# Performance work log

Measured on AMD Instinct MI355X. Metric: run time of the kernel, lower is better.

## Reference

```python
import jax, jax.numpy as jnp
import numpy as np

B, S, DIM, H, D = 2, 2048, 1024, 16, 64
WINDOW = 512
MAX_MEM_SEGMENTS = 1
ROPE_THETA = 10000.0


def _rope(t, pos):
    # lucidrains rotary-embedding-torch default: interleaved pairs
    d = t.shape[-1]
    inv_freq = 1.0 / (ROPE_THETA ** (jnp.arange(0, d, 2, dtype=jnp.float32) / d))
    freqs = pos[:, None].astype(jnp.float32) * inv_freq[None, :]        # [S, d/2]
    freqs = jnp.repeat(freqs, 2, axis=-1)                               # [S, d]
    cos, sin = jnp.cos(freqs), jnp.sin(freqs)
    t1, t2 = t[..., 0::2], t[..., 1::2]
    rot = jnp.stack((-t2, t1), axis=-1).reshape(t.shape)                # rotate_half
    return t * cos + rot * sin


def setup_inputs() -> dict:
    key = jax.random.key(0)
    ks = jax.random.split(key, 8)
    tokens = jax.random.normal(ks[0], (B, S, DIM), dtype=jnp.float32)
    value_residual = jax.random.normal(ks[1], (B, H, S, D), dtype=jnp.float32)
    episode_ids = jnp.sort(jax.random.randint(ks[2], (B, S), 0, 4), axis=-1)
    w = 0.02
    Wq = jax.random.normal(ks[3], (DIM, H * D), dtype=jnp.float32) * w
    Wkv = jax.random.normal(ks[4], (DIM, 2 * H * D), dtype=jnp.float32) * w
    Wo = jax.random.normal(ks[5], (H * D, DIM), dtype=jnp.float32) * w
    Wg = jax.random.normal(ks[6], (DIM, H), dtype=jnp.float32) * w
    Wmix = jax.random.normal(ks[7], (DIM, H), dtype=jnp.float32) * w
    return {"tokens": tokens, "value_residual": value_residual, "episode_ids": episode_ids,
            "Wq": Wq, "Wkv": Wkv, "Wo": Wo, "Wg": Wg, "Wmix": Wmix}


def reference(tokens, value_residual, episode_ids, Wq, Wkv, Wo, Wg, Wmix):
    b, s, _ = tokens.shape
    scale = D ** -0.5

    def split_heads(x):  # [b, n, h*d] -> [b, h, n, d]
        return x.reshape(b, s, H, D).transpose(0, 2, 1, 3)

    q = split_heads(tokens @ Wq)
    kv = tokens @ Wkv
    k, v = split_heads(kv[..., :H * D]), split_heads(kv[..., H * D:])

    q = q * scale

    # value-residual lerp: v.lerp(value_residual, mix)
    mix = jax.nn.sigmoid(jnp.einsum('bnd,dh->bhn', tokens, Wmix))[..., None]  # [b,h,n,1]
    v = v + mix * (value_residual - v)

    pos = jnp.arange(s)
    q = _rope(q, pos)
    k = _rope(k, pos)

    sim = jnp.einsum('bhid,bhjd->bhij', q, k)

    # fixed-window causal mask: masked where dist < 0 or dist > max_mem_segments*window
    dist = pos[:, None] - pos[None, :]
    win_mask = (dist < 0) | (dist > MAX_MEM_SEGMENTS * WINDOW)            # [s, s]
    ep_mask = episode_ids[:, :, None] != episode_ids[:, None, :]          # [b, s, s]
    mask = win_mask[None, None, :, :] | ep_mask[:, None, :, :]

    sim = jnp.where(mask, -jnp.finfo(sim.dtype).max, sim)
    attn = jax.nn.softmax(sim, axis=-1)
    out = jnp.einsum('bhij,bhjd->bhid', attn, v)

    # sigmoid value gating
    gate = jax.nn.sigmoid(jnp.einsum('bnd,dh->bhn', tokens, Wg))[..., None]
    out = out * gate

    out = out.transpose(0, 2, 1, 3).reshape(b, s, H * D)
    return out @ Wo
```

## Files before the change

### kernel.cpp

```cpp
#include <hip/hip_runtime.h>
#include <math.h>

#define BB 2
#define SS 2048
#define DIMM 1024
#define HH 16
#define DD 64
#define WINDOW 512

typedef __bf16 bf16x8 __attribute__((ext_vector_type(8)));
typedef __bf16 bf16x4 __attribute__((ext_vector_type(4)));
typedef float f32x4 __attribute__((ext_vector_type(4)));

__device__ __forceinline__ unsigned short f2bf(float f) {
    unsigned int u = __float_as_uint(f);
    u = (u + 0x7FFFu + ((u >> 16) & 1u)) >> 16;
    return (unsigned short)u;
}
__device__ __forceinline__ float bf2f(unsigned short u) {
    return __uint_as_float((unsigned int)u << 16);
}

__device__ __forceinline__ void async_cp16(unsigned short* lds_dst, const unsigned short* g_src) {
    __builtin_amdgcn_global_load_lds(
        (const __attribute__((address_space(1))) unsigned int*)g_src,
        (__attribute__((address_space(3))) unsigned int*)lds_dst, 16, 0, 0);
}

__global__ __launch_bounds__(256) void prep_kernel(
    const float* __restrict__ tokens, unsigned short* __restrict__ tokA,
    const float* __restrict__ Wg, const float* __restrict__ Wmix,
    unsigned short* __restrict__ wgmt,
    const int* __restrict__ ep, int* __restrict__ epstart)
{
    int bid = blockIdx.x;
    int tid = threadIdx.x;
    if (bid < 2048) {
        const int n4 = (BB * SS * DIMM) / 4;
        for (int i = bid * 256 + tid; i < n4; i += 2048 * 256) {
            float4 v = ((const float4*)tokens)[i];
            ushort4 o;
            o.x = f2bf(v.x); o.y = f2bf(v.y); o.z = f2bf(v.z); o.w = f2bf(v.w);
            ((ushort4*)tokA)[i] = o;
        }
    } else if (bid < 2176) {
        int idx = (bid - 2048) * 256 + tid;
        int n = idx >> 10, k = idx & 1023;
        const float* src = (n < 16) ? Wg : Wmix;
        wgmt[idx] = f2bf(src[k * HH + (n & 15)]);
    } else {
        int idx = (bid - 2176) * 256 + tid;
        int b = idx >> 11, i = idx & 2047;
        const int* e = ep + b * SS;
        int v = e[i];
        int lo = 0, hi = i;
        while (lo < hi) {
            int mid = (lo + hi) >> 1;
            if (e[mid] == v) hi = mid; else lo = mid + 1;
        }
        epstart[idx] = lo;
    }
}

__global__ __launch_bounds__(256) void transpose_cvt3_kernel(
    const float* __restrict__ Wq, const float* __restrict__ Wkv,
    const float* __restrict__ Wo, unsigned short* __restrict__ BtW,
    unsigned short* __restrict__ WotW)
{
    int z = blockIdx.z;
    const float* src = (z == 0) ? Wq : (z == 1) ? Wkv : Wo;
    unsigned short* dst = (z == 0) ? BtW : (z == 1) ? (BtW + 1024 * 1024) : WotW;
    int C = (z == 1) ? 2048 : 1024;
    if (blockIdx.x * 32 >= C) return;
    const int R = 1024;

    __shared__ float t[32][33];
    int c0 = blockIdx.x * 32, r0 = blockIdx.y * 32;
    int tx = threadIdx.x & 31, ty = threadIdx.x >> 5;
    #pragma unroll
    for (int u = 0; u < 4; ++u)
        t[ty + 8 * u][tx] = src[(size_t)(r0 + ty + 8 * u) * C + c0 + tx];
    __syncthreads();
    #pragma unroll
    for (int u = 0; u < 4; ++u)
        dst[(size_t)(c0 + ty + 8 * u) * R + r0 + tx] = f2bf(t[tx][ty + 8 * u]);
}

__global__ __launch_bounds__(256) void mixgate_mfma(
    const unsigned short* __restrict__ A,
    const unsigned short* __restrict__ Bt,
    float* __restrict__ gate, float* __restrict__ mix)
{
    int mbase = blockIdx.x * 16;
    int tid = threadIdx.x;
    int wave = tid >> 6, lane = tid & 63;
    int fr = lane & 15, hi = lane >> 4;
    int kw = wave * 256;

    __shared__ float red[4][16][32];

    f32x4 acc[2];
    acc[0] = (f32x4){0.f, 0.f, 0.f, 0.f};
    acc[1] = (f32x4){0.f, 0.f, 0.f, 0.f};

    const unsigned short* a0 = A + (size_t)(mbase + fr) * 1024 + kw + hi * 8;
    const unsigned short* b0 = Bt + (size_t)fr * 1024 + kw + hi * 8;
    const unsigned short* b1 = Bt + (size_t)(16 + fr) * 1024 + kw + hi * 8;

    #pragma unroll 2
    for (int k = 0; k < 256; k += 32) {
        bf16x8 af0 = *(const bf16x8*)(a0 + k);
        bf16x8 bf0 = *(const bf16x8*)(b0 + k);
        bf16x8 bf1 = *(const bf16x8*)(b1 + k);
        acc[0] = __builtin_amdgcn_mfma_f32_16x16x32_bf16(af0, bf0, acc[0], 0, 0, 0);
        acc[1] = __builtin_amdgcn_mfma_f32_16x16x32_bf16(af0, bf1, acc[1], 0, 0, 0);
    }

    #pragma unroll
    for (int n_ = 0; n_ < 2; ++n_)
        #pragma unroll
        for (int j = 0; j < 4; ++j)
            red[wave][hi * 4 + j][n_ * 16 + fr] = acc[n_][j];
    __syncthreads();

    #pragma unroll
    for (int e = 0; e < 2; ++e) {
        int idx = tid * 2 + e;
        int r = idx >> 5, c = idx & 31;
        float s4 = red[0][r][c] + red[1][r][c] + red[2][r][c] + red[3][r][c];
        float sg = 1.f / (1.f + __expf(-s4));
        int mg = mbase + r;
        int b = mg >> 11, s = mg & 2047;
        int h = c & 15;
        float* dst = (c < 16) ? gate : mix;
        dst[((size_t)b * HH + h) * SS + s] = sg;
    }
}

template<int EPI, int BM, int BN>
__global__ __launch_bounds__(256) void gemm_mfma(
    const unsigned short* __restrict__ A, const unsigned short* __restrict__ Bt,
    void* __restrict__ o0v, void* __restrict__ o1v, void* __restrict__ o2v)
{
    const int K = 1024;
    constexpr int MFR = BM / 32;
    constexpr int NFR = BN / 32;
    int nbase = blockIdx.x * BN;
    int mbase = blockIdx.y * BM;

    int tid = threadIdx.x;
    int lane = tid & 63;
    int wave = tid >> 6;
    int wr = wave >> 1, wc = wave & 1;
    int fr = lane & 15, hi = lane >> 4;

    __shared__ unsigned short As[2][BM * 32];
    __shared__ unsigned short Bs[2][BN * 32];

    int srow = tid >> 2;
    int sp   = tid & 3;
    int scol = (sp ^ ((srow >> 1) & 3)) * 8;
    const unsigned short* agp0 = A  + (size_t)(mbase + srow) * K + scol;
    const unsigned short* agp1 = (BM == 128)
        ? A + (size_t)(mbase + srow + 64) * K + scol : agp0;
    const unsigned short* bgp0 = Bt + (size_t)(nbase + srow) * K + scol;
    const unsigned short* bgp1 = (BN == 128)
        ? Bt + (size_t)(nbase + srow + 64) * K + scol : bgp0;

    f32x4 acc[MFR][NFR];
    #pragma unroll
    for (int m_ = 0; m_ < MFR; ++m_)
        #pragma unroll
        for (int n_ = 0; n_ < NFR; ++n_)
            acc[m_][n_] = (f32x4){0.f, 0.f, 0.f, 0.f};

    int aidx[MFR], bidx[NFR];
    #pragma unroll
    for (int m_ = 0; m_ < MFR; ++m_) {
        int row = wr * (BM / 2) + m_ * 16 + fr;
        aidx[m_] = row * 32 + (hi ^ ((row >> 1) & 3)) * 8;
    }
    #pragma unroll
    for (int n_ = 0; n_ < NFR; ++n_) {
        int row = wc * (BN / 2) + n_ * 16 + fr;
        bidx[n_] = row * 32 + (hi ^ ((row >> 1) & 3)) * 8;
    }

    auto stage = [&](int buf, int k0) {
        async_cp16(&As[buf][tid * 8], agp0 + k0);
        if constexpr (BM == 128)
            async_cp16(&As[buf][2048 + tid * 8], agp1 + k0);
        async_cp16(&Bs[buf][tid * 8], bgp0 + k0);
        if constexpr (BN == 128)
            async_cp16(&Bs[buf][2048 + tid * 8], bgp1 + k0);
    };

    stage(0, 0);
    for (int k0 = 0; k0 < K; k0 += 32) {
        int cur = (k0 >> 5) & 1;
        __syncthreads();
        if (k0 + 32 < K) stage(cur ^ 1, k0 + 32);

        bf16x8 af[MFR], bfr[NFR];
        #pragma unroll
        for (int m_ = 0; m_ < MFR; ++m_) af[m_] = *(const bf16x8*)&As[cur][aidx[m_]];
        #pragma unroll
        for (int n_ = 0; n_ < NFR; ++n_) bfr[n_] = *(const bf16x8*)&Bs[cur][bidx[n_]];
        #pragma unroll
        for (int m_ = 0; m_ < MFR; ++m_)
            #pragma unroll
            for (int n_ = 0; n_ < NFR; ++n_)
                acc[m_][n_] = __builtin_amdgcn_mfma_f32_16x16x32_bf16(
                    af[m_], bfr[n_], acc[m_][n_], 0, 0, 0);
    }

    #pragma unroll
    for (int m_ = 0; m_ < MFR; ++m_) {
        #pragma unroll
        for (int n_ = 0; n_ < NFR; ++n_) {
            int c = nbase + wc * (BN / 2) + n_ * 16 + fr;
            #pragma unroll
            for (int j = 0; j < 4; ++j) {
                int mg = mbase + wr * (BM / 2) + m_ * 16 + hi * 4 + j;
                float v = acc[m_][n_][j];
                if (EPI == 0) {
                    ((float*)o0v)[(size_t)mg * 1024 + c] = v;
                } else {
                    int b = mg >> 11, s = mg & 2047;
                    int cc = c & 1023, h = cc >> 6, d = cc & 63;
                    unsigned short* dst = (c < 1024) ? (unsigned short*)o0v
                                        : (c < 2048) ? (unsigned short*)o1v
                                                     : (unsigned short*)o2v;
                    dst[(((size_t)b * HH + h) * SS + s) * DD + d] = f2bf(v);
                }
            }
        }
    }
}

__global__ __launch_bounds__(256) void rope_lerp_kernel(
    unsigned short* __restrict__ q, unsigned short* __restrict__ k,
    const unsigned short* __restrict__ v0, const float* __restrict__ vres,
    const float* __restrict__ mix, unsigned short* __restrict__ vt)
{
    int st = blockIdx.x;
    int bh = blockIdx.y;
    int tid = threadIdx.x;
    int sl = tid >> 2;
    int dg = (tid & 3) * 16;
    int s = st * 64 + sl;
    size_t rowoff = ((size_t)bh * SS + s) * DD + dg;

    __shared__ unsigned short vtile[64][66];

    union { uint4 v[2]; unsigned short u[16]; } qa, ka, va;
    qa.v[0] = *(const uint4*)(q + rowoff);
    qa.v[1] = *(const uint4*)(q + rowoff + 8);
    ka.v[0] = *(const uint4*)(k + rowoff);
    ka.v[1] = *(const uint4*)(k + rowoff + 8);
    va.v[0] = *(const uint4*)(v0 + rowoff);
    va.v[1] = *(const uint4*)(v0 + rowoff + 8);
    float4 w[4];
    #pragma unroll
    for (int u = 0; u < 4; ++u) w[u] = *(const float4*)(vres + rowoff + 4 * u);
    float mx = mix[(size_t)bh * SS + s];

    #pragma unroll
    for (int u = 0; u < 8; ++u) {
        int d0 = dg + 2 * u;
        float inv_freq = powf(10000.f, -(float)d0 * (1.f / 64.f));
        float fr = (float)s * inv_freq;
        float red = fr - 6.2831853f * floorf(fr * 0.15915494f);
        float cs, sn;
        __sincosf(red, &sn, &cs);
        float x = bf2f(qa.u[2 * u]), y = bf2f(qa.u[2 * u + 1]);
        qa.u[2 * u]     = f2bf((x * cs - y * sn) * 0.125f);
        qa.u[2 * u + 1] = f2bf((y * cs + x * sn) * 0.125f);
        x = bf2f(ka.u[2 * u]); y = bf2f(ka.u[2 * u + 1]);
        ka.u[2 * u]     = f2bf(x * cs - y * sn);
        ka.u[2 * u + 1] = f2bf(y * cs + x * sn);
    }
    *(uint4*)(q + rowoff)     = qa.v[0];
    *(uint4*)(q + rowoff + 8) = qa.v[1];
    *(uint4*)(k + rowoff)     = ka.v[0];
    *(uint4*)(k + rowoff + 8) = ka.v[1];

    #pragma unroll
    for (int e = 0; e < 16; ++e) {
        float vv = bf2f(va.u[e]);
        float wr = ((const float*)w)[e];
        vtile[sl][dg + e] = f2bf(vv + mx * (wr - vv));
    }
    __syncthreads();

    int d = tid >> 2;
    int sseg = (tid & 3) * 16;
    union { uint4 v[2]; unsigned short u[16]; } ot;
    #pragma unroll
    for (int e = 0; e < 16; ++e) ot.u[e] = vtile[sseg + e][d];
    unsigned short* dst = vt + ((size_t)bh * DD + d) * SS + st * 64 + sseg;
    *(uint4*)dst = ot.v[0];
    *(uint4*)(dst + 8) = ot.v[1];
}

__global__ __launch_bounds__(256) void attn_mfma(
    const unsigned short* __restrict__ qbh, const unsigned short* __restrict__ kbh,
    const unsigned short* __restrict__ vt, const int* __restrict__ epstart,
    const float* __restrict__ gate, unsigned short* __restrict__ ao)
{
    int orig = blockIdx.x;
    int swz  = (orig & 7) * 128 + (orig >> 3);
    int bh = swz >> 5, qt = swz & 31;
    int b = bh >> 4, h = bh & 15;
    int q0 = qt * 64;
    int tid = threadIdx.x;
    int wave = tid >> 6, lane = tid & 63;
    int lq = lane & 15, lg = lane >> 4;
    int i = q0 + wave * 16 + lq;

    __shared__ unsigned short Ks[4096];
    __shared__ unsigned short Vs[4096];
    alignas(16) __shared__ unsigned short P_lds[4][16][72];

    int srow0 = tid >> 3, sch = tid & 7;
    int srow1 = srow0 + 32;
    int sc0 = ((sch ^ (srow0 & 7)) << 3);
    int sc1 = ((sch ^ (srow1 & 7)) << 3);
    const unsigned short* kS0 = kbh + ((size_t)bh * SS + srow0) * DD + sc0;
    const unsigned short* kS1 = kbh + ((size_t)bh * SS + srow1) * DD + sc1;
    const unsigned short* vS0 = vt + ((size_t)bh * DD + srow0) * SS + sc0;
    const unsigned short* vS1 = vt + ((size_t)bh * DD + srow1) * SS + sc1;

    int fidx[4];
    #pragma unroll
    for (int n = 0; n < 4; ++n) {
        int r = 16 * n + lq;
        fidx[n] = r * 64 + ((lg ^ (r & 7)) << 3);
    }

    const unsigned short* qrow = qbh + ((size_t)bh * SS + i) * DD + lg * 8;
    bf16x8 bq0 = *(const bf16x8*)qrow;
    bf16x8 bq1 = *(const bf16x8*)(qrow + 32);

    int jmin = i - WINDOW;
    int es = epstart[b * SS + i];
    if (es > jmin) jmin = es;
    float gi = gate[(size_t)bh * SS + i];

    float m = -1e30f, l = 0.f;
    f32x4 o[4];
    #pragma unroll
    for (int n = 0; n < 4; ++n) o[n] = (f32x4){0.f, 0.f, 0.f, 0.f};

    int t0 = (qt < 8) ? (8 - qt) : 0;
    int nt = 9 - t0;
    int jb0 = 64 * (qt - 8 + t0);

    for (int u = 0; u < nt; ++u) {
        int jbase = jb0 + 64 * u;

        __syncthreads();
        async_cp16(&Ks[tid * 8],        kS0 + (size_t)jbase * DD);
        async_cp16(&Ks[2048 + tid * 8], kS1 + (size_t)jbase * DD);
        async_cp16(&Vs[tid * 8],        vS0 + jbase);
        async_cp16(&Vs[2048 + tid * 8], vS1 + jbase);
        __syncthreads();

        f32x4 acc[4];
        #pragma unroll
        for (int n = 0; n < 4; ++n) acc[n] = (f32x4){0.f, 0.f, 0.f, 0.f};
        __builtin_amdgcn_s_setprio(1);
        #pragma unroll
        for (int n = 0; n < 4; ++n) {
            bf16x8 kf0 = *(const bf16x8*)&Ks[fidx[n]];
            bf16x8 kf1 = *(const bf16x8*)&Ks[fidx[n] ^ 32];
            acc[n] = __builtin_amdgcn_mfma_f32_16x16x32_bf16(kf0, bq0, acc[n], 0, 0, 0);
            acc[n] = __builtin_amdgcn_mfma_f32_16x16x32_bf16(kf1, bq1, acc[n], 0, 0, 0);
        }
        __builtin_amdgcn_s_setprio(0);

        int jb = jbase + lg * 4;
        #pragma unroll
        for (int n = 0; n < 4; ++n)
            #pragma unroll
            for (int r = 0; r < 4; ++r) {
                int j = jb + 16 * n + r;
                if (j < jmin || j > i) acc[n][r] = -3e38f;
            }

        float tm = -3e38f;
        #pragma unroll
        for (int n = 0; n < 4; ++n)
            tm = fmaxf(tm, fmaxf(fmaxf(acc[n][0], acc[n][1]), fmaxf(acc[n][2], acc[n][3])));
        tm = fmaxf(tm, __shfl_xor(tm, 16, 64));
        tm = fmaxf(tm, __shfl_xor(tm, 32, 64));
        float mnew = fmaxf(m, tm);
        float scale = __expf(m - mnew);
        float ts = 0.f;
        #pragma unroll
        for (int n = 0; n < 4; ++n)
            #pragma unroll
            for (int r = 0; r < 4; ++r) {
                float p = __expf(acc[n][r] - mnew);
                acc[n][r] = p;
                ts += p;
            }
        ts += __shfl_xor(ts, 16, 64);
        ts += __shfl_xor(ts, 32, 64);
        l = l * scale + ts;
        m = mnew;
        #pragma unroll
        for (int n = 0; n < 4; ++n) o[n] = o[n] * scale;

        #pragma unroll
        for (int n = 0; n < 4; ++n) {
            bf16x4 pv;
            pv[0] = (__bf16)acc[n][0]; pv[1] = (__bf16)acc[n][1];
            pv[2] = (__bf16)acc[n][2]; pv[3] = (__bf16)acc[n][3];
            *(bf16x4*)&P_lds[wave][lq][16 * n + lg * 4] = pv;
        }
        bf16x8 bp0 = *(const bf16x8*)&P_lds[wave][lq][lg * 8];
        bf16x8 bp1 = *(const bf16x8*)&P_lds[wave][lq][32 + lg * 8];

        __builtin_amdgcn_s_setprio(1);
        #pragma unroll
        for (int n = 0; n < 4; ++n) {
            bf16x8 vf0 = *(const bf16x8*)&Vs[fidx[n]];
            bf16x8 vf1 = *(const bf16x8*)&Vs[fidx[n] ^ 32];
            o[n] = __builtin_amdgcn_mfma_f32_16x16x32_bf16(vf0, bp0, o[n], 0, 0, 0);
            o[n] = __builtin_amdgcn_mfma_f32_16x16x32_bf16(vf1, bp1, o[n], 0, 0, 0);
        }
        __builtin_amdgcn_s_setprio(0);
    }

    float g = gi / l;
    #pragma unroll
    for (int n = 0; n < 4; ++n) {
        bf16x4 ov;
        ov[0] = (__bf16)(o[n][0] * g); ov[1] = (__bf16)(o[n][1] * g);
        ov[2] = (__bf16)(o[n][2] * g); ov[3] = (__bf16)(o[n][3] * g);
        *(bf16x4*)(ao + (((size_t)b * SS + i) * HH + h) * DD + 16 * n + lg * 4) = ov;
    }
}

extern "C" void kernel_launch(void* const* d_in, const int* in_sizes, int n_in,
                              void* d_out, int out_size, void* d_ws, size_t ws_size,
                              hipStream_t stream)
{
    const float* tokens = (const float*)d_in[0];
    const float* vres   = (const float*)d_in[1];
    const int*   ep     = (const int*)d_in[2];
    const float* Wq     = (const float*)d_in[3];
    const float* Wkv    = (const float*)d_in[4];
    const float* Wo     = (const float*)d_in[5];
    const float* Wg     = (const float*)d_in[6];
    const float* Wmix   = (const float*)d_in[7];
    float* out = (float*)d_out;

    char* wsb = (char*)d_ws;
    unsigned short* qbh  = (unsigned short*)(wsb + 0);
    unsigned short* kbh  = (unsigned short*)(wsb + 8388608);
    unsigned short* vb0  = (unsigned short*)(wsb + 16777216);
    unsigned short* vtb  = (unsigned short*)(wsb + 25165824);
    unsigned short* aob  = (unsigned short*)(wsb + 33554432);
    unsigned short* tokA = (unsigned short*)(wsb + 41943040);
    unsigned short* BtW  = (unsigned short*)(wsb + 50331648);
    float* gatep = (float*)(wsb + 56623104);
    float* mixp  = (float*)(wsb + 56885248);
    int*   epst  = (int*)(wsb + 57147392);
    unsigned short* wgmt = (unsigned short*)(wsb + 57163776);
    unsigned short* WotW = (unsigned short*)(wsb + 57229312);

    prep_kernel<<<2192, 256, 0, stream>>>(tokens, tokA, Wg, Wmix, wgmt, ep, epst);
    transpose_cvt3_kernel<<<dim3(64, 32, 3), 256, 0, stream>>>(Wq, Wkv, Wo, BtW, WotW);

    mixgate_mfma<<<256, 256, 0, stream>>>(tokA, wgmt, gatep, mixp);
    gemm_mfma<1, 128, 128><<<dim3(24, 32), 256, 0, stream>>>(tokA, BtW, qbh, kbh, vb0);
    rope_lerp_kernel<<<dim3(SS / 64, BB * HH), 256, 0, stream>>>(qbh, kbh, vb0, vres, mixp, vtb);
    attn_mfma<<<1024, 256, 0, stream>>>(qbh, kbh, vtb, epst, gatep, aob);

    gemm_mfma<0, 128, 64><<<dim3(16, 32), 256, 0, stream>>>(aob, WotW, out, nullptr, nullptr);
}
```

Measured before the change: 117.8 us.

## Add dedicated 256x256-tile QKV projection GEMM with swizzled LDS and block remap

Replaces the generic 128x128 GEMM for the QKV projection with a specialized 512-thread kernel that uses 256x256 output tiles, K-steps of 64, and an XOR-swizzled LDS layout to avoid bank conflicts. It also remaps block indices so neighbouring blocks share operand tiles in cache, and double-buffers async global-to-LDS loads with explicit vmcnt waits. The generic GEMM loses its QKV epilogue and is kept only for the output projection. Larger tiles raise data reuse but launch only 192 blocks and use about 128KB of LDS and many accumulator registers, which may cut occupancy and leave some compute units idle on a 256-CU part.

```diff
diff --git a/kernel.cpp b/kernel.cpp
--- a/kernel.cpp
+++ b/kernel.cpp
@@ -137,10 +137,117 @@
     }
 }
 
-template<int EPI, int BM, int BN>
+__global__ __launch_bounds__(512) void gemm_proj256(
+    const unsigned short* __restrict__ A, const unsigned short* __restrict__ Bt,
+    unsigned short* __restrict__ q, unsigned short* __restrict__ kbuf,
+    unsigned short* __restrict__ v)
+{
+    const int K = 1024;
+    const int NT = 16;
+
+    int lin = blockIdx.y * 12 + blockIdx.x;
+    int swz = (lin & 7) * 24 + (lin >> 3);
+    int nbase = (swz % 12) * 256;
+    int mbase = (swz / 12) * 256;
+
+    int tid = threadIdx.x;
+    int lane = tid & 63;
+    int wave = tid >> 6;
+    int wr = wave >> 2, wc = wave & 3;
+    int fr = lane & 15, hi = lane >> 4;
+
+    __shared__ unsigned short As[2][256 * 64];
+    __shared__ unsigned short Bs[2][256 * 64];
+
+    int srow_in = tid >> 3;
+    int g_ch = (lane & 7) ^ (lane >> 3);
+
+    auto stage = [&](int buf, int kt) {
+        int k0 = kt * 64;
+        #pragma unroll
+        for (int s = 0; s < 4; ++s) {
+            int row = s * 64 + srow_in;
+            async_cp16(&As[buf][s * 4096 + tid * 8],
+                       A + (size_t)(mbase + row) * K + k0 + g_ch * 8);
+        }
+        #pragma unroll
+        for (int s = 0; s < 4; ++s) {
+            int row = s * 64 + srow_in;
+            async_cp16(&Bs[buf][s * 4096 + tid * 8],
+                       Bt + (size_t)(nbase + row) * K + k0 + g_ch * 8);
+        }
+    };
+
+    f32x4 acc[8][4];
+    #pragma unroll
+    for (int mf = 0; mf < 8; ++mf)
+        #pragma unroll
+        for (int nf = 0; nf < 4; ++nf)
+            acc[mf][nf] = (f32x4){0.f, 0.f, 0.f, 0.f};
+
+    int sofs0 = ((0 * 4 + hi) ^ (fr & 7)) * 8;
+    int sofs1 = ((1 * 4 + hi) ^ (fr & 7)) * 8;
+    int arow0 = (wr * 128 + fr) * 64;
+    int brow0 = (wc * 64 + fr) * 64;
+
+    auto compute = [&](int buf) {
+        #pragma unroll
+        for (int ks = 0; ks < 2; ++ks) {
+            int so = ks ? sofs1 : sofs0;
+            bf16x8 bfr[4];
+            #pragma unroll
+            for (int nf = 0; nf < 4; ++nf)
+                bfr[nf] = *(const bf16x8*)&Bs[buf][brow0 + nf * 1024 + so];
+            #pragma unroll
+            for (int mf = 0; mf < 8; ++mf) {
+                bf16x8 af = *(const bf16x8*)&As[buf][arow0 + mf * 1024 + so];
+                #pragma unroll
+                for (int nf = 0; nf < 4; ++nf)
+                    acc[mf][nf] = __builtin_amdgcn_mfma_f32_16x16x32_bf16(
+                        af, bfr[nf], acc[mf][nf], 0, 0, 0);
+            }
+        }
+    };
+
+    stage(0, 0);
+    stage(1, 1);
+    for (int kt = 0; kt < NT; kt += 2) {
+        if (kt + 1 < NT) asm volatile("s_waitcnt vmcnt(8)" ::: "memory");
+        else             asm volatile("s_waitcnt vmcnt(0)" ::: "memory");
+        __builtin_amdgcn_s_barrier();
+        compute(0);
+        __builtin_amdgcn_s_barrier();
+        if (kt + 2 < NT) stage(0, kt + 2);
+
+        if (kt + 2 < NT) asm volatile("s_waitcnt vmcnt(8)" ::: "memory");
+        else             asm volatile("s_waitcnt vmcnt(0)" ::: "memory");
+        __builtin_amdgcn_s_barrier();
+        compute(1);
+        __builtin_amdgcn_s_barrier();
+        if (kt + 3 < NT) stage(1, kt + 3);
+    }
+
+    #pragma unroll
+    for (int mf = 0; mf < 8; ++mf) {
+        #pragma unroll
+        for (int nf = 0; nf < 4; ++nf) {
+            int c = nbase + wc * 64 + nf * 16 + fr;
+            int cc = c & 1023, h = cc >> 6, d = cc & 63;
+            unsigned short* dst = (c < 1024) ? q : (c < 2048) ? kbuf : v;
+            #pragma unroll
+            for (int j = 0; j < 4; ++j) {
+                int mg = mbase + wr * 128 + mf * 16 + hi * 4 + j;
+                int b = mg >> 11, s = mg & 2047;
+                dst[(((size_t)b * HH + h) * SS + s) * DD + d] = f2bf(acc[mf][nf][j]);
+            }
+        }
+    }
+}
+
+template<int BM, int BN>
 __global__ __launch_bounds__(256) void gemm_mfma(
     const unsigned short* __restrict__ A, const unsigned short* __restrict__ Bt,
-    void* __restrict__ o0v, void* __restrict__ o1v, void* __restrict__ o2v)
+    float* __restrict__ C)
 {
     const int K = 1024;
     constexpr int MFR = BM / 32;
@@ -222,17 +329,7 @@
             #pragma unroll
             for (int j = 0; j < 4; ++j) {
                 int mg = mbase + wr * (BM / 2) + m_ * 16 + hi * 4 + j;
-                float v = acc[m_][n_][j];
-                if (EPI == 0) {
-                    ((float*)o0v)[(size_t)mg * 1024 + c] = v;
-                } else {
-                    int b = mg >> 11, s = mg & 2047;
-                    int cc = c & 1023, h = cc >> 6, d = cc & 63;
-                    unsigned short* dst = (c < 1024) ? (unsigned short*)o0v
-                                        : (c < 2048) ? (unsigned short*)o1v
-                                                     : (unsigned short*)o2v;
-                    dst[(((size_t)b * HH + h) * SS + s) * DD + d] = f2bf(v);
-                }
+                C[(size_t)mg * 1024 + c] = acc[m_][n_][j];
             }
         }
     }
@@ -475,9 +572,9 @@
     transpose_cvt3_kernel<<<dim3(64, 32, 3), 256, 0, stream>>>(Wq, Wkv, Wo, BtW, WotW);
 
     mixgate_mfma<<<256, 256, 0, stream>>>(tokA, wgmt, gatep, mixp);
-    gemm_mfma<1, 128, 128><<<dim3(24, 32), 256, 0, stream>>>(tokA, BtW, qbh, kbh, vb0);
+    gemm_proj256<<<dim3(12, 16), 512, 0, stream>>>(tokA, BtW, qbh, kbh, vb0);
     rope_lerp_kernel<<<dim3(SS / 64, BB * HH), 256, 0, stream>>>(qbh, kbh, vb0, vres, mixp, vtb);
     attn_mfma<<<1024, 256, 0, stream>>>(qbh, kbh, vtb, epst, gatep, aob);
 
-    gemm_mfma<0, 128, 64><<<dim3(16, 32), 256, 0, stream>>>(aob, WotW, out, nullptr, nullptr);
-}
+    gemm_mfma<128, 64><<<dim3(16, 32), 256, 0, stream>>>(aob, WotW, out);
+}
```

Result: no change. 118.5 us (+0.6%).

## Merge prep kernels, fuse mix/gate into QKV GEMM, widen attention blocks

Applied to the files above, without the earlier changes.

Folds the weight transpose/convert kernel into the token prep kernel, and merges the mix/gate projection into the QKV projection GEMM launch as extra blocks. This cuts two kernel launches and lets the small mixgate work fill idle slots next to the GEMM tiles. Attention blocks grow to 128 query rows with 512 threads, so each K/V tile loaded into LDS is shared by twice as many queries, at the cost of fewer blocks and a wider causal key range per block.

```diff
diff --git a/kernel.cpp b/kernel.cpp
--- a/kernel.cpp
+++ b/kernel.cpp
@@ -27,29 +27,56 @@
         (__attribute__((address_space(3))) unsigned int*)lds_dst, 16, 0, 0);
 }
 
-__global__ __launch_bounds__(256) void prep_kernel(
+__global__ __launch_bounds__(256) void prep_all_kernel(
     const float* __restrict__ tokens, unsigned short* __restrict__ tokA,
+    const float* __restrict__ Wq, const float* __restrict__ Wkv,
+    const float* __restrict__ Wo, unsigned short* __restrict__ BtW,
+    unsigned short* __restrict__ WotW,
     const float* __restrict__ Wg, const float* __restrict__ Wmix,
     unsigned short* __restrict__ wgmt,
     const int* __restrict__ ep, int* __restrict__ epstart)
 {
     int bid = blockIdx.x;
     int tid = threadIdx.x;
-    if (bid < 2048) {
+    if (bid < 4096) {
+        const float* src;
+        unsigned short* dst;
+        int C, bx, by;
+        if (bid < 1024) {
+            src = Wq; dst = BtW; C = 1024; bx = bid & 31; by = bid >> 5;
+        } else if (bid < 3072) {
+            int rel = bid - 1024;
+            src = Wkv; dst = BtW + 1024 * 1024; C = 2048; bx = rel & 63; by = rel >> 6;
+        } else {
+            int rel = bid - 3072;
+            src = Wo; dst = WotW; C = 1024; bx = rel & 31; by = rel >> 5;
+        }
+        const int R = 1024;
+        __shared__ float t[32][33];
+        int c0 = bx * 32, r0 = by * 32;
+        int tx = tid & 31, ty = tid >> 5;
+        #pragma unroll
+        for (int u = 0; u < 4; ++u)
+            t[ty + 8 * u][tx] = src[(size_t)(r0 + ty + 8 * u) * C + c0 + tx];
+        __syncthreads();
+        #pragma unroll
+        for (int u = 0; u < 4; ++u)
+            dst[(size_t)(c0 + ty + 8 * u) * R + r0 + tx] = f2bf(t[tx][ty + 8 * u]);
+    } else if (bid < 6144) {
         const int n4 = (BB * SS * DIMM) / 4;
-        for (int i = bid * 256 + tid; i < n4; i += 2048 * 256) {
+        for (int i = (bid - 4096) * 256 + tid; i < n4; i += 2048 * 256) {
             float4 v = ((const float4*)tokens)[i];
             ushort4 o;
             o.x = f2bf(v.x); o.y = f2bf(v.y); o.z = f2bf(v.z); o.w = f2bf(v.w);
             ((ushort4*)tokA)[i] = o;
         }
-    } else if (bid < 2176) {
-        int idx = (bid - 2048) * 256 + tid;
+    } else if (bid < 6272) {
+        int idx = (bid - 6144) * 256 + tid;
         int n = idx >> 10, k = idx & 1023;
         const float* src = (n < 16) ? Wg : Wmix;
         wgmt[idx] = f2bf(src[k * HH + (n & 15)]);
     } else {
-        int idx = (bid - 2176) * 256 + tid;
+        int idx = (bid - 6272) * 256 + tid;
         int b = idx >> 11, i = idx & 2047;
         const int* e = ep + b * SS;
         int v = e[i];
@@ -62,85 +89,144 @@
     }
 }
 
-__global__ __launch_bounds__(256) void transpose_cvt3_kernel(
-    const float* __restrict__ Wq, const float* __restrict__ Wkv,
-    const float* __restrict__ Wo, unsigned short* __restrict__ BtW,
-    unsigned short* __restrict__ WotW)
-{
-    int z = blockIdx.z;
-    const float* src = (z == 0) ? Wq : (z == 1) ? Wkv : Wo;
-    unsigned short* dst = (z == 0) ? BtW : (z == 1) ? (BtW + 1024 * 1024) : WotW;
-    int C = (z == 1) ? 2048 : 1024;
-    if (blockIdx.x * 32 >= C) return;
-    const int R = 1024;
-
-    __shared__ float t[32][33];
-    int c0 = blockIdx.x * 32, r0 = blockIdx.y * 32;
-    int tx = threadIdx.x & 31, ty = threadIdx.x >> 5;
-    #pragma unroll
-    for (int u = 0; u < 4; ++u)
-        t[ty + 8 * u][tx] = src[(size_t)(r0 + ty + 8 * u) * C + c0 + tx];
-    __syncthreads();
-    #pragma unroll
-    for (int u = 0; u < 4; ++u)
-        dst[(size_t)(c0 + ty + 8 * u) * R + r0 + tx] = f2bf(t[tx][ty + 8 * u]);
-}
-
-__global__ __launch_bounds__(256) void mixgate_mfma(
-    const unsigned short* __restrict__ A,
-    const unsigned short* __restrict__ Bt,
+__global__ __launch_bounds__(256) void projmix_kernel(
+    const unsigned short* __restrict__ A, const unsigned short* __restrict__ Bt,
+    unsigned short* __restrict__ qo, unsigned short* __restrict__ ko,
+    unsigned short* __restrict__ vo,
+    const unsigned short* __restrict__ wgmt,
     float* __restrict__ gate, float* __restrict__ mix)
 {
-    int mbase = blockIdx.x * 16;
+    __shared__ unsigned short As[2][128 * 32];
+    __shared__ unsigned short Bs[2][128 * 32];
+    __shared__ float red[4][16][32];
+
+    const int K = 1024;
+    int bid = blockIdx.x;
     int tid = threadIdx.x;
-    int wave = tid >> 6, lane = tid & 63;
+    int lane = tid & 63;
+    int wave = tid >> 6;
     int fr = lane & 15, hi = lane >> 4;
-    int kw = wave * 256;
-
-    __shared__ float red[4][16][32];
-
-    f32x4 acc[2];
-    acc[0] = (f32x4){0.f, 0.f, 0.f, 0.f};
-    acc[1] = (f32x4){0.f, 0.f, 0.f, 0.f};
-
-    const unsigned short* a0 = A + (size_t)(mbase + fr) * 1024 + kw + hi * 8;
-    const unsigned short* b0 = Bt + (size_t)fr * 1024 + kw + hi * 8;
-    const unsigned short* b1 = Bt + (size_t)(16 + fr) * 1024 + kw + hi * 8;
-
-    #pragma unroll 2
-    for (int k = 0; k < 256; k += 32) {
-        bf16x8 af0 = *(const bf16x8*)(a0 + k);
-        bf16x8 bf0 = *(const bf16x8*)(b0 + k);
-        bf16x8 bf1 = *(const bf16x8*)(b1 + k);
-        acc[0] = __builtin_amdgcn_mfma_f32_16x16x32_bf16(af0, bf0, acc[0], 0, 0, 0);
-        acc[1] = __builtin_amdgcn_mfma_f32_16x16x32_bf16(af0, bf1, acc[1], 0, 0, 0);
-    }
-
-    #pragma unroll
-    for (int n_ = 0; n_ < 2; ++n_)
-        #pragma unroll
-        for (int j = 0; j < 4; ++j)
-            red[wave][hi * 4 + j][n_ * 16 + fr] = acc[n_][j];
-    __syncthreads();
-
-    #pragma unroll
-    for (int e = 0; e < 2; ++e) {
-        int idx = tid * 2 + e;
-        int r = idx >> 5, c = idx & 31;
-        float s4 = red[0][r][c] + red[1][r][c] + red[2][r][c] + red[3][r][c];
-        float sg = 1.f / (1.f + __expf(-s4));
-        int mg = mbase + r;
-        int b = mg >> 11, s = mg & 2047;
-        int h = c & 15;
-        float* dst = (c < 16) ? gate : mix;
-        dst[((size_t)b * HH + h) * SS + s] = sg;
-    }
-}
-
-template<int EPI, int BM, int BN>
+
+    if (bid < 768) {
+        int nbase = (bid % 24) * 128;
+        int mbase = (bid / 24) * 128;
+        int wr = wave >> 1, wc = wave & 1;
+
+        int srow = tid >> 2;
+        int sp   = tid & 3;
+        int scol = (sp ^ ((srow >> 1) & 3)) * 8;
+        const unsigned short* agp0 = A  + (size_t)(mbase + srow) * K + scol;
+        const unsigned short* agp1 = A  + (size_t)(mbase + srow + 64) * K + scol;
+        const unsigned short* bgp0 = Bt + (size_t)(nbase + srow) * K + scol;
+        const unsigned short* bgp1 = Bt + (size_t)(nbase + srow + 64) * K + scol;
+
+        f32x4 acc[4][4];
+        #pragma unroll
+        for (int m_ = 0; m_ < 4; ++m_)
+            #pragma unroll
+            for (int n_ = 0; n_ < 4; ++n_)
+                acc[m_][n_] = (f32x4){0.f, 0.f, 0.f, 0.f};
+
+        int aidx[4], bidx[4];
+        #pragma unroll
+        for (int m_ = 0; m_ < 4; ++m_) {
+            int row = wr * 64 + m_ * 16 + fr;
+            aidx[m_] = row * 32 + (hi ^ ((row >> 1) & 3)) * 8;
+        }
+        #pragma unroll
+        for (int n_ = 0; n_ < 4; ++n_) {
+            int row = wc * 64 + n_ * 16 + fr;
+            bidx[n_] = row * 32 + (hi ^ ((row >> 1) & 3)) * 8;
+        }
+
+        auto stage = [&](int buf, int k0) {
+            async_cp16(&As[buf][tid * 8], agp0 + k0);
+            async_cp16(&As[buf][2048 + tid * 8], agp1 + k0);
+            async_cp16(&Bs[buf][tid * 8], bgp0 + k0);
+            async_cp16(&Bs[buf][2048 + tid * 8], bgp1 + k0);
+        };
+
+        stage(0, 0);
+        for (int k0 = 0; k0 < K; k0 += 32) {
+            int cur = (k0 >> 5) & 1;
+            __syncthreads();
+            if (k0 + 32 < K) stage(cur ^ 1, k0 + 32);
+
+            bf16x8 af[4], bfr[4];
+            #pragma unroll
+            for (int m_ = 0; m_ < 4; ++m_) af[m_] = *(const bf16x8*)&As[cur][aidx[m_]];
+            #pragma unroll
+            for (int n_ = 0; n_ < 4; ++n_) bfr[n_] = *(const bf16x8*)&Bs[cur][bidx[n_]];
+            #pragma unroll
+            for (int m_ = 0; m_ < 4; ++m_)
+                #pragma unroll
+                for (int n_ = 0; n_ < 4; ++n_)
+                    acc[m_][n_] = __builtin_amdgcn_mfma_f32_16x16x32_bf16(
+                        af[m_], bfr[n_], acc[m_][n_], 0, 0, 0);
+        }
+
+        #pragma unroll
+        for (int m_ = 0; m_ < 4; ++m_) {
+            #pragma unroll
+            for (int n_ = 0; n_ < 4; ++n_) {
+                int c = nbase + wc * 64 + n_ * 16 + fr;
+                int cc = c & 1023, h = cc >> 6, d = cc & 63;
+                unsigned short* dst = (c < 1024) ? qo : (c < 2048) ? ko : vo;
+                #pragma unroll
+                for (int j = 0; j < 4; ++j) {
+                    int mg = mbase + wr * 64 + m_ * 16 + hi * 4 + j;
+                    int b = mg >> 11, s = mg & 2047;
+                    dst[(((size_t)b * HH + h) * SS + s) * DD + d] = f2bf(acc[m_][n_][j]);
+                }
+            }
+        }
+    } else {
+        int mbase = (bid - 768) * 16;
+        int kw = wave * 256;
+
+        f32x4 acc[2];
+        acc[0] = (f32x4){0.f, 0.f, 0.f, 0.f};
+        acc[1] = (f32x4){0.f, 0.f, 0.f, 0.f};
+
+        const unsigned short* a0 = A + (size_t)(mbase + fr) * 1024 + kw + hi * 8;
+        const unsigned short* b0 = wgmt + (size_t)fr * 1024 + kw + hi * 8;
+        const unsigned short* b1 = wgmt + (size_t)(16 + fr) * 1024 + kw + hi * 8;
+
+        #pragma unroll 2
+        for (int k = 0; k < 256; k += 32) {
+            bf16x8 af0 = *(const bf16x8*)(a0 + k);
+            bf16x8 bf0 = *(const bf16x8*)(b0 + k);
+            bf16x8 bf1 = *(const bf16x8*)(b1 + k);
+            acc[0] = __builtin_amdgcn_mfma_f32_16x16x32_bf16(af0, bf0, acc[0], 0, 0, 0);
+            acc[1] = __builtin_amdgcn_mfma_f32_16x16x32_bf16(af0, bf1, acc[1], 0, 0, 0);
+        }
+
+        #pragma unroll
+        for (int n_ = 0; n_ < 2; ++n_)
+            #pragma unroll
+            for (int j = 0; j < 4; ++j)
+                red[wave][hi * 4 + j][n_ * 16 + fr] = acc[n_][j];
+        __syncthreads();
+
+        #pragma unroll
+        for (int e = 0; e < 2; ++e) {
+            int idx = tid * 2 + e;
+            int r = idx >> 5, c = idx & 31;
+            float s4 = red[0][r][c] + red[1][r][c] + red[2][r][c] + red[3][r][c];
+            float sg = 1.f / (1.f + __expf(-s4));
+            int mg = mbase + r;
+            int b = mg >> 11, s = mg & 2047;
+            int h = c & 15;
+            float* dst = (c < 16) ? gate : mix;
+            dst[((size_t)b * HH + h) * SS + s] = sg;
+        }
+    }
+}
+
+template<int BM, int BN>
 __global__ __launch_bounds__(256) void gemm_mfma(
     const unsigned short* __restrict__ A, const unsigned short* __restrict__ Bt,
-    void* __restrict__ o0v, void* __restrict__ o1v, void* __restrict__ o2v)
+    float* __restrict__ C)
 {
     const int K = 1024;
     constexpr int MFR = BM / 32;
@@ -222,17 +308,7 @@
             #pragma unroll
             for (int j = 0; j < 4; ++j) {
                 int mg = mbase + wr * (BM / 2) + m_ * 16 + hi * 4 + j;
-                float v = acc[m_][n_][j];
-                if (EPI == 0) {
-                    ((float*)o0v)[(size_t)mg * 1024 + c] = v;
-                } else {
-                    int b = mg >> 11, s = mg & 2047;
-                    int cc = c & 1023, h = cc >> 6, d = cc & 63;
-                    unsigned short* dst = (c < 1024) ? (unsigned short*)o0v
-                                        : (c < 2048) ? (unsigned short*)o1v
-                                                     : (unsigned short*)o2v;
-                    dst[(((size_t)b * HH + h) * SS + s) * DD + d] = f2bf(v);
-                }
+                C[(size_t)mg * 1024 + c] = acc[m_][n_][j];
             }
         }
     }
@@ -303,16 +379,16 @@
     *(uint4*)(dst + 8) = ot.v[1];
 }
 
-__global__ __launch_bounds__(256) void attn_mfma(
+__global__ __launch_bounds__(512) void attn_mfma(
     const unsigned short* __restrict__ qbh, const unsigned short* __restrict__ kbh,
     const unsigned short* __restrict__ vt, const int* __restrict__ epstart,
     const float* __restrict__ gate, unsigned short* __restrict__ ao)
 {
     int orig = blockIdx.x;
-    int swz  = (orig & 7) * 128 + (orig >> 3);
-    int bh = swz >> 5, qt = swz & 31;
+    int swz  = (orig & 7) * 64 + (orig >> 3);
+    int bh = swz >> 4, qt = swz & 15;
     int b = bh >> 4, h = bh & 15;
-    int q0 = qt * 64;
+    int q0 = qt * 128;
     int tid = threadIdx.x;
     int wave = tid >> 6, lane = tid & 63;
     int lq = lane & 15, lg = lane >> 4;
@@ -320,16 +396,12 @@
 
     __shared__ unsigned short Ks[4096];
     __shared__ unsigned short Vs[4096];
-    alignas(16) __shared__ unsigned short P_lds[4][16][72];
-
-    int srow0 = tid >> 3, sch = tid & 7;
-    int srow1 = srow0 + 32;
-    int sc0 = ((sch ^ (srow0 & 7)) << 3);
-    int sc1 = ((sch ^ (srow1 & 7)) << 3);
-    const unsigned short* kS0 = kbh + ((size_t)bh * SS + srow0) * DD + sc0;
-    const unsigned short* kS1 = kbh + ((size_t)bh * SS + srow1) * DD + sc1;
-    const unsigned short* vS0 = vt + ((size_t)bh * DD + srow0) * SS + sc0;
-    const unsigned short* vS1 = vt + ((size_t)bh * DD + srow1) * SS + sc1;
+    alignas(16) __shared__ unsigned short P_lds[8][16][72];
+
+    int srow = tid >> 3;
+    int sc = (((tid & 7) ^ (srow & 7)) << 3);
+    const unsigned short* kS = kbh + ((size_t)bh * SS + srow) * DD + sc;
+    const unsigned short* vS = vt + ((size_t)bh * DD + srow) * SS + sc;
 
     int fidx[4];
     #pragma unroll
@@ -352,18 +424,17 @@
     #pragma unroll
     for (int n = 0; n < 4; ++n) o[n] = (f32x4){0.f, 0.f, 0.f, 0.f};
 
-    int t0 = (qt < 8) ? (8 - qt) : 0;
-    int nt = 9 - t0;
-    int jb0 = 64 * (qt - 8 + t0);
+    int jt0 = (q0 >= 512) ? ((q0 - 512) >> 6) : 0;
+    int jt1 = (q0 + 127) >> 6;
+    int nt = jt1 - jt0 + 1;
+    int jb0 = jt0 * 64;
 
     for (int u = 0; u < nt; ++u) {
         int jbase = jb0 + 64 * u;
 
         __syncthreads();
-        async_cp16(&Ks[tid * 8],        kS0 + (size_t)jbase * DD);
-        async_cp16(&Ks[2048 + tid * 8], kS1 + (size_t)jbase * DD);
-        async_cp16(&Vs[tid * 8],        vS0 + jbase);
-        async_cp16(&Vs[2048 + tid * 8], vS1 + jbase);
+        async_cp16(&Ks[tid * 8], kS + (size_t)jbase * DD);
+        async_cp16(&Vs[tid * 8], vS + jbase);
         __syncthreads();
 
         f32x4 acc[4];
@@ -471,13 +542,12 @@
     unsigned short* wgmt = (unsigned short*)(wsb + 57163776);
     unsigned short* WotW = (unsigned short*)(wsb + 57229312);
 
-    prep_kernel<<<2192, 256, 0, stream>>>(tokens, tokA, Wg, Wmix, wgmt, ep, epst);
-    transpose_cvt3_kernel<<<dim3(64, 32, 3), 256, 0, stream>>>(Wq, Wkv, Wo, BtW, WotW);
-
-    mixgate_mfma<<<256, 256, 0, stream>>>(tokA, wgmt, gatep, mixp);
-    gemm_mfma<1, 128, 128><<<dim3(24, 32), 256, 0, stream>>>(tokA, BtW, qbh, kbh, vb0);
+    prep_all_kernel<<<6288, 256, 0, stream>>>(tokens, tokA, Wq, Wkv, Wo, BtW, WotW,
+                                              Wg, Wmix, wgmt, ep, epst);
+    projmix_kernel<<<1024, 256, 0, stream>>>(tokA, BtW, qbh, kbh, vb0,
+                                             wgmt, gatep, mixp);
     rope_lerp_kernel<<<dim3(SS / 64, BB * HH), 256, 0, stream>>>(qbh, kbh, vb0, vres, mixp, vtb);
-    attn_mfma<<<1024, 256, 0, stream>>>(qbh, kbh, vtb, epst, gatep, aob);
-
-    gemm_mfma<0, 128, 64><<<dim3(16, 32), 256, 0, stream>>>(aob, WotW, out, nullptr, nullptr);
-}
+    attn_mfma<<<512, 512, 0, stream>>>(qbh, kbh, vtb, epst, gatep, aob);
+
+    gemm_mfma<128, 64><<<dim3(16, 32), 256, 0, stream>>>(aob, WotW, out);
+}
```

Result: faster. 113.9 us (-3.3%).
